# Kernel tuning notes

Measured on AMD Instinct MI355X. Metric: run time of the kernel, lower is better.

## Reference

```python
import jax, jax.numpy as jnp
import numpy as np

HEADS, DH, DIM = 16, 64, 1024
GAMMA, LAMBDA_REG = 0.01, 0.001


def _ln(x, g, b, eps=1e-5):
    mu = x.mean(-1, keepdims=True)
    var = x.var(-1, keepdims=True)  # biased var, matches torch LayerNorm
    return (x - mu) / jnp.sqrt(var + eps) * g + b


def setup_inputs() -> dict:
    key = jax.random.key(0)
    ks = jax.random.split(key, 8)
    B, NQ, NK = 8, 512, 512
    inner = HEADS * DH
    rn = lambda i, shp, sc: jax.random.normal(ks[i], shp, jnp.float32) * sc
    return {
        "q": rn(0, (B, NQ, DIM), 1.0),
        "k": rn(1, (B, NK, DIM), 1.0),
        "v": rn(2, (B, NK, DIM), 1.0),
        "ln_g": jnp.ones((DIM,), jnp.float32),
        "ln_b": jnp.zeros((DIM,), jnp.float32),
        "w_in": rn(3, (DIM, inner), 0.02),
        "wp_w1": rn(4, (2 * DH, DH), 0.05),
        "wp_b1": jnp.zeros((DH,), jnp.float32),
        "wp_lng": jnp.ones((DH,), jnp.float32),
        "wp_lnb": jnp.zeros((DH,), jnp.float32),
        "wp_w2": rn(5, (DH, DH // 2), 0.05),
        "wp_b2": jnp.zeros((DH // 2,), jnp.float32),
        "wp_w3": rn(6, (DH // 2, 3), 0.05),
        "wp_b3": jnp.zeros((3,), jnp.float32),
        "w_temp": jnp.ones((1,), jnp.float32) * 0.8,
        "w_out": rn(7, (inner, DIM), 0.02),
        "b_out": jnp.zeros((DIM,), jnp.float32),
    }


def reference(q, k, v, ln_g, ln_b, w_in, wp_w1, wp_b1, wp_lng, wp_lnb,
              wp_w2, wp_b2, wp_w3, wp_b3, w_temp, w_out, b_out):
    sg = jax.lax.stop_gradient

    def proj(x):  # input_linear (dropout=identity in eval) + head split
        y = _ln(x, ln_g, ln_b) @ w_in                      # [B,N,inner]
        B, N, _ = y.shape
        return y.reshape(B, N, HEADS, DH).transpose(2, 0, 1, 3)  # [h,B,N,d]

    f_q, f_k, f_v = proj(q), proj(k), proj(v)
    m = f_k.shape[2]
    eps = 1e-8

    # --- cosine component (clamp applied twice, as in source) ---
    dots = jnp.einsum('hbnd,hbmd->hbnm', f_q, f_k)
    n1 = jnp.linalg.norm(f_q, axis=-1, keepdims=True) + eps   # [h,B,Nq,1]
    n2 = jnp.linalg.norm(f_k, axis=-1, keepdims=True) + eps   # [h,B,Nk,1]
    cosine_sim = jnp.clip(dots / (n1 * jnp.swapaxes(n2, -1, -2)), -0.98, 0.98)

    # --- regularized covariance component ---
    f_kc = f_k - f_k.mean(axis=2, keepdims=True)
    f_qc = f_q - f_q.mean(axis=-1, keepdims=True)
    cov = jnp.einsum('hbnd,hbmd->hbnm', f_qc, f_kc) / (DH ** 0.5 + 1e-6)
    health = jnp.std(cov, ddof=1)
    base = LAMBDA_REG / max(m, 1)
    reg = jnp.where(health < 1e-5, base * 5.0,
                    jnp.where(health < 1e-3, base * 2.0, base))
    cov = jnp.clip(reg * cov, -25.0, 25.0)

    # --- margin-based variance component (eval: adaptive_gamma = gamma) ---
    fqn = f_q / jnp.maximum(jnp.linalg.norm(f_q, axis=-1, keepdims=True), 1e-6)
    fkn = f_k / jnp.maximum(jnp.linalg.norm(f_k, axis=-1, keepdims=True), 1e-6)
    cs = jnp.clip(jnp.einsum('hbnd,hbmd->hbnm', fqn, fkn), -0.98, 0.98)
    margin = jnp.clip(GAMMA - cs, 0.0, 5.0)
    var_c = jnp.broadcast_to(margin.mean(-1, keepdims=True), cs.shape)

    # --- dynamic per-head weight predictor MLP ---
    qk = jnp.concatenate([f_q.mean(axis=(1, 2)), f_k.mean(axis=(1, 2))], -1)  # [h,2d]
    h1 = jax.nn.relu(_ln(qk @ wp_w1 + wp_b1, wp_lng, wp_lnb))
    h2 = jax.nn.relu(h1 @ wp_w2 + wp_b2)
    logits = jax.nn.softmax(h2 @ wp_w3 + wp_b3, -1)  # MLP ends in Softmax
    temp = jnp.clip(w_temp, 0.1, 5.0)
    w = jax.nn.softmax(logits / temp, -1)            # second softmax with temp
    w = jnp.clip(w, 0.08, 0.75)
    w = w / w.sum(-1, keepdims=True)
    cw = w[:, 0].reshape(HEADS, 1, 1, 1)
    covw = w[:, 1].reshape(HEADS, 1, 1, 1)
    varw = w[:, 2].reshape(HEADS, 1, 1, 1)

    # --- health-based normalization (stds detached, as in source) ---
    cn = sg(jnp.std(cosine_sim, ddof=1)) + 1e-6
    covn = sg(jnp.std(cov, ddof=1)) + 1e-6
    varn = sg(jnp.std(var_c, ddof=1)) + 1e-6
    ch = jnp.minimum(cn, 1.0)
    covh = jnp.minimum(covn * 10.0, 1.0)
    varh = jnp.minimum(varn * 10.0, 1.0)
    dots_f = (cw * (cosine_sim / cn * ch)
              + covw * (cov / covn * 0.4 * covh)
              + varw * (var_c / varn * 0.4 * varh))

    # --- diversity-adaptive softmax temperature ---
    div = jnp.std(dots_f, ddof=1)
    atemp = jnp.where(div < 1e-5, 0.05, jnp.where(div < 1e-3, 0.2, 0.5 + div))
    atemp = jnp.clip(atemp, 0.05, 2.0)
    attn = jax.nn.softmax(dots_f / atemp, axis=-1)

    out = jnp.einsum('hbnm,hbmd->hbnd', attn, f_v)
    out = out.transpose(1, 2, 0, 3).reshape(q.shape[0], q.shape[1], HEADS * DH)
    return out @ w_out + b_out  # output_linear (dropout=identity)
```

## Files before the change

### kernel.cpp

```cpp
#include <hip/hip_runtime.h>
#include <math.h>

#define NHEADS 16
#define DHEAD  64
#define NDIM   1024
#define NB     8
#define NSEQ   512
#define NROWS  4096
#define NHB    128
#define NTOTD  33554432.0

typedef __bf16 bf16x8 __attribute__((ext_vector_type(8)));
typedef __bf16 bf16x4 __attribute__((ext_vector_type(4)));
typedef float  f32x4  __attribute__((ext_vector_type(4)));

#define MFMA(a,b,c) __builtin_amdgcn_mfma_f32_16x16x32_bf16(a,b,c,0,0,0)

static __device__ __forceinline__ size_t qk_off(int hbq, int n, int d){
  return ((size_t)hbq*32 + (n>>4))*1024 + (size_t)(d>>3)*128 + (size_t)(n&15)*8 + (d&7);
}

#define O_DSUMH  0
#define O_DSUME  1024
#define O_SCAL   2048
#define O_COEF   3072
#define O_W      4096
#define O_RQ1    131072
#define O_RQ2    393216
#define O_MQ     655360
#define O_QDMK   917504
#define O_RK1    1179648
#define O_RK2    1441792
#define O_KS2    1703936
#define O_MARG   1966080
#define O_RCS    2228224
#define O_RCOV   2490368
#define O_MK     2752512
#define O_QCOL   2785280
#define O_QHI    4194304
#define O_QLO    12582912
#define O_KHI    20971520
#define O_KLO    29360128
#define O_VTH    37748736
#define O_VTL    46137344
#define O_LNST   54525952
#define O_WTH    71303168
#define O_WTL    73400320
#define O_OUTH   75497472
#define O_OUTL   83886080
#define O_WOTH   92274688
#define O_WOTL   94371840

static __device__ __forceinline__ float clamp98(float x){ return fminf(fmaxf(x,-0.98f),0.98f); }

__global__ __launch_bounds__(256) void ln_stats_kernel(const float* __restrict__ q,
    const float* __restrict__ k, const float* __restrict__ v, float* __restrict__ st){
  int row = blockIdx.x, t = threadIdx.x;
  const float* x = (blockIdx.y==0) ? q : (blockIdx.y==1 ? k : v);
  float4 vv = *(const float4*)(x + (size_t)row*1024 + t*4);
  float s  = vv.x+vv.y+vv.z+vv.w;
  float ss = vv.x*vv.x+vv.y*vv.y+vv.z*vv.z+vv.w*vv.w;
  for (int off=32; off; off>>=1){ s += __shfl_down(s,off); ss += __shfl_down(ss,off); }
  __shared__ float sh[8];
  if ((t&63)==0){ sh[t>>6]=s; sh[4+(t>>6)]=ss; }
  __syncthreads();
  if (t==0){
    float S=sh[0]+sh[1]+sh[2]+sh[3], SS=sh[4]+sh[5]+sh[6]+sh[7];
    float mu = S*(1.0f/1024.0f);
    st[blockIdx.y*8192 + row*2]   = mu;
    st[blockIdx.y*8192 + row*2+1] = 1.0f/sqrtf(SS*(1.0f/1024.0f) - mu*mu + 1e-5f);
  }
}

__global__ __launch_bounds__(256) void transpose_split_kernel(const float* __restrict__ wsrc,
    __bf16* __restrict__ th, __bf16* __restrict__ tl){
  __shared__ float tile[64][65];
  int k0 = blockIdx.x*64, n0 = blockIdx.y*64;
  int t = threadIdx.x;
  int c = t&63, r4 = t>>6;
  #pragma unroll
  for (int i=0;i<16;i++){
    int kr = r4 + i*4;
    tile[kr][c] = wsrc[(size_t)(k0+kr)*1024 + n0 + c];
  }
  __syncthreads();
  #pragma unroll
  for (int i=0;i<16;i++){
    int nr = r4 + i*4;
    float v = tile[c][nr];
    __bf16 hv = (__bf16)v;
    size_t o = (size_t)(n0+nr)*1024 + k0 + c;
    th[o] = hv; tl[o] = (__bf16)(v - (float)hv);
  }
}

__global__ __launch_bounds__(256) void proj_gemm_kernel(
  const float* __restrict__ q, const float* __restrict__ k, const float* __restrict__ v,
  const float* __restrict__ lnst0,
  const float* __restrict__ gv, const float* __restrict__ bv,
  const __bf16* __restrict__ Bth, const __bf16* __restrict__ Btl,
  __bf16* __restrict__ qhi, __bf16* __restrict__ qlo,
  __bf16* __restrict__ khi, __bf16* __restrict__ klo,
  __bf16* __restrict__ vth, __bf16* __restrict__ vtl)
{
  __shared__ __bf16 Ash[128][68];
  __shared__ __bf16 Asl[128][68];
  __shared__ __bf16 Bsh[64][68];
  __shared__ __bf16 Bsl[64][68];
  int z = blockIdx.z;
  const float* X = (z==0)? q : (z==1? k : v);
  const float* lnst = lnst0 + z*8192;
  __bf16* oh = (z==0)? qhi : (z==1? khi : vth);
  __bf16* ol = (z==0)? qlo : (z==1? klo : vtl);
  int t = threadIdx.x, w = t>>6, lane = t&63, lr = lane&15, lq = lane>>4;
  int vid = blockIdx.y*16 + blockIdx.x;
  int cX = vid&7, r2 = vid>>3;
  int ytile = cX*4 + (r2>>4);
  int xtile = r2&15;
  int rbase = ytile*128;
  int cbase = xtile*64;
  int wr = w>>1, wc = w&1;
  int srow = t>>3;
  int scol = (t&7)*8;
  f32x4 acc[4][2] = {};
  for (int kt=0; kt<16; kt++){
    int k0 = kt*64;
    bf16x8 va[4], vA[4], vb[2], vB[2];
    float4 g0 = *(const float4*)(gv + k0 + scol);
    float4 g1 = *(const float4*)(gv + k0 + scol + 4);
    float4 b0 = *(const float4*)(bv + k0 + scol);
    float4 b1 = *(const float4*)(bv + k0 + scol + 4);
    #pragma unroll
    for (int r=0;r<4;r++){
      int row = rbase + r*32 + srow;
      size_t gi = (size_t)row*1024 + k0 + scol;
      float4 x0 = *(const float4*)(X + gi);
      float4 x1 = *(const float4*)(X + gi + 4);
      float mu = lnst[row*2], rs = lnst[row*2+1];
      float o[8];
      o[0]=(x0.x-mu)*rs*g0.x+b0.x; o[1]=(x0.y-mu)*rs*g0.y+b0.y;
      o[2]=(x0.z-mu)*rs*g0.z+b0.z; o[3]=(x0.w-mu)*rs*g0.w+b0.w;
      o[4]=(x1.x-mu)*rs*g1.x+b1.x; o[5]=(x1.y-mu)*rs*g1.y+b1.y;
      o[6]=(x1.z-mu)*rs*g1.z+b1.z; o[7]=(x1.w-mu)*rs*g1.w+b1.w;
      bf16x8 hv, lv;
      #pragma unroll
      for (int e=0;e<8;e++){
        __bf16 hb_ = (__bf16)o[e];
        hv[e] = hb_; lv[e] = (__bf16)(o[e]-(float)hb_);
      }
      va[r]=hv; vA[r]=lv;
    }
    #pragma unroll
    for (int r=0;r<2;r++){
      size_t gi = (size_t)(cbase + r*32 + srow)*1024 + k0 + scol;
      vb[r] = *(const bf16x8*)(Bth + gi);
      vB[r] = *(const bf16x8*)(Btl + gi);
    }
    #pragma unroll
    for (int r=0;r<4;r++){
      *(bf16x8*)&Ash[r*32+srow][scol] = va[r];
      *(bf16x8*)&Asl[r*32+srow][scol] = vA[r];
    }
    #pragma unroll
    for (int r=0;r<2;r++){
      *(bf16x8*)&Bsh[r*32+srow][scol] = vb[r];
      *(bf16x8*)&Bsl[r*32+srow][scol] = vB[r];
    }
    __syncthreads();
    #pragma unroll
    for (int kc=0; kc<2; kc++){
      int ko = kc*32 + lq*8;
      bf16x8 ah[4], al[4], bh[2], bl[2];
      #pragma unroll
      for (int i=0;i<4;i++){
        ah[i] = *(const bf16x8*)&Ash[wr*64 + i*16 + lr][ko];
        al[i] = *(const bf16x8*)&Asl[wr*64 + i*16 + lr][ko];
      }
      #pragma unroll
      for (int j=0;j<2;j++){
        bh[j] = *(const bf16x8*)&Bsh[wc*32 + j*16 + lr][ko];
        bl[j] = *(const bf16x8*)&Bsl[wc*32 + j*16 + lr][ko];
      }
      #pragma unroll
      for (int i=0;i<4;i++)
        #pragma unroll
        for (int j=0;j<2;j++){
          acc[i][j] = MFMA(al[i], bh[j], acc[i][j]);
          acc[i][j] = MFMA(ah[i], bl[j], acc[i][j]);
          acc[i][j] = MFMA(ah[i], bh[j], acc[i][j]);
        }
    }
    __syncthreads();
  }
  #pragma unroll
  for (int i=0;i<4;i++)
    #pragma unroll
    for (int j=0;j<2;j++)
      #pragma unroll
      for (int r=0;r<4;r++){
        int row = rbase + wr*64 + i*16 + lq*4 + r;
        int col = cbase + wc*32 + j*16 + lr;
        float val = acc[i][j][r];
        __bf16 hv = (__bf16)val;
        __bf16 lv = (__bf16)(val - (float)hv);
        int n = row & 511, b2 = row >> 9;
        int hh = col >> 6, d = col & 63;
        int hbq = hh*8 + b2;
        size_t o;
        if (z<2){
          o = qk_off(hbq, n, d);
        } else {
          o = (((size_t)hbq*4 + (d>>4))*16 + (n>>5))*512
            + (size_t)((((n>>3)&3)*16) + (d&15))*8 + (n&7);
        }
        oh[o] = hv; ol[o] = lv;
      }
}

__global__ __launch_bounds__(256) void final_gemm_kernel(
  const __bf16* __restrict__ Ah, const __bf16* __restrict__ Al,
  const __bf16* __restrict__ Bth, const __bf16* __restrict__ Btl,
  const float* __restrict__ bias, float* __restrict__ of)
{
  __shared__ __bf16 Ash[128][68];
  __shared__ __bf16 Asl[128][68];
  __shared__ __bf16 Bsh[64][68];
  __shared__ __bf16 Bsl[64][68];
  int t = threadIdx.x, w = t>>6, lane = t&63, lr = lane&15, lq = lane>>4;
  int vid = blockIdx.y*16 + blockIdx.x;
  int cX = vid&7, r2 = vid>>3;
  int ytile = cX*4 + (r2>>4);
  int xtile = r2&15;
  int rbase = ytile*128;
  int cbase = xtile*64;
  int wr = w>>1, wc = w&1;
  int srow = t>>3;
  int scol = (t&7)*8;
  f32x4 acc[4][2] = {};
  for (int kt=0; kt<16; kt++){
    int k0 = kt*64;
    bf16x8 va[4], vA[4], vb[2], vB[2];
    #pragma unroll
    for (int r=0;r<4;r++){
      size_t gi = (size_t)(rbase + r*32 + srow)*1024 + k0 + scol;
      va[r] = *(const bf16x8*)(Ah + gi);
      vA[r] = *(const bf16x8*)(Al + gi);
    }
    #pragma unroll
    for (int r=0;r<2;r++){
      size_t gi = (size_t)(cbase + r*32 + srow)*1024 + k0 + scol;
      vb[r] = *(const bf16x8*)(Bth + gi);
      vB[r] = *(const bf16x8*)(Btl + gi);
    }
    #pragma unroll
    for (int r=0;r<4;r++){
      *(bf16x8*)&Ash[r*32+srow][scol] = va[r];
      *(bf16x8*)&Asl[r*32+srow][scol] = vA[r];
    }
    #pragma unroll
    for (int r=0;r<2;r++){
      *(bf16x8*)&Bsh[r*32+srow][scol] = vb[r];
      *(bf16x8*)&Bsl[r*32+srow][scol] = vB[r];
    }
    __syncthreads();
    #pragma unroll
    for (int kc=0; kc<2; kc++){
      int ko = kc*32 + lq*8;
      bf16x8 ah[4], al[4], bh[2], bl[2];
      #pragma unroll
      for (int i=0;i<4;i++){
        ah[i] = *(const bf16x8*)&Ash[wr*64 + i*16 + lr][ko];
        al[i] = *(const bf16x8*)&Asl[wr*64 + i*16 + lr][ko];
      }
      #pragma unroll
      for (int j=0;j<2;j++){
        bh[j] = *(const bf16x8*)&Bsh[wc*32 + j*16 + lr][ko];
        bl[j] = *(const bf16x8*)&Bsl[wc*32 + j*16 + lr][ko];
      }
      #pragma unroll
      for (int i=0;i<4;i++)
        #pragma unroll
        for (int j=0;j<2;j++){
          acc[i][j] = MFMA(al[i], bh[j], acc[i][j]);
          acc[i][j] = MFMA(ah[i], bl[j], acc[i][j]);
          acc[i][j] = MFMA(ah[i], bh[j], acc[i][j]);
        }
    }
    __syncthreads();
  }
  #pragma unroll
  for (int i=0;i<4;i++)
    #pragma unroll
    for (int j=0;j<2;j++)
      #pragma unroll
      for (int r=0;r<4;r++){
        int row = rbase + wr*64 + i*16 + lq*4 + r;
        int col = cbase + wc*32 + j*16 + lr;
        of[(size_t)row*1024 + col] = acc[i][j][r] + bias[col];
      }
}

__global__ void kstats_kernel(const __bf16* __restrict__ kh, const __bf16* __restrict__ kl,
    float* __restrict__ mk, float* __restrict__ rk1, float* __restrict__ rk2, float* __restrict__ ks2){
  int hb = blockIdx.x;
  size_t base = (size_t)hb*32768;
  int t = threadIdx.x;
  __shared__ float csA[32][64];
  __shared__ float mks_lds[64];
  __shared__ float mksum_sh;
  int c2 = t&7, mg = t>>3;
  float fs[8] = {};
  for (int m=mg; m<512; m+=32){
    size_t off = base + (size_t)(m>>4)*1024 + c2*128 + (size_t)(m&15)*8;
    bf16x8 h = *(const bf16x8*)(kh+off);
    bf16x8 l = *(const bf16x8*)(kl+off);
    #pragma unroll
    for (int e=0;e<8;e++) fs[e] += (float)h[e]+(float)l[e];
  }
  #pragma unroll
  for (int e=0;e<8;e++) csA[mg][c2*8+e] = fs[e];
  __syncthreads();
  if (t<64){
    float s=0;
    #pragma unroll
    for (int g=0;g<32;g++) s += csA[g][t];
    float vv = s*(1.0f/512.0f);
    mk[hb*64+t] = vv;
    mks_lds[t] = vv;
  }
  __syncthreads();
  if (t==0){
    float s=0;
    for (int i=0;i<64;i++) s += mks_lds[i];
    mksum_sh = s;
  }
  __syncthreads();
  float mks = mksum_sh;
  int l8 = t&7, rg = t>>3;
  for (int m=rg; m<512; m+=32){
    size_t off = base + (size_t)(m>>4)*1024 + l8*128 + (size_t)(m&15)*8;
    bf16x8 h = *(const bf16x8*)(kh+off);
    bf16x8 l = *(const bf16x8*)(kl+off);
    float s=0, ss=0;
    #pragma unroll
    for (int e=0;e<8;e++){ float vv=(float)h[e]+(float)l[e]; s+=vv; ss+=vv*vv; }
    for (int o2=4;o2;o2>>=1){ s+=__shfl_xor(s,o2); ss+=__shfl_xor(ss,o2); }
    if (l8==0){
      float nk = sqrtf(ss);
      rk1[hb*512+m] = 1.0f/(nk+1e-8f);
      rk2[hb*512+m] = 1.0f/fmaxf(nk,1e-6f);
      ks2[hb*512+m] = s - mks;
    }
  }
}

__global__ void qstats_kernel(const __bf16* __restrict__ qh, const __bf16* __restrict__ ql,
    const float* __restrict__ mk, float* __restrict__ rq1, float* __restrict__ rq2,
    float* __restrict__ mq, float* __restrict__ qdotmk, float* __restrict__ qcol){
  int hb = blockIdx.x;
  size_t base = (size_t)hb*32768;
  int t = threadIdx.x;
  __shared__ float csA[32][64];
  __shared__ float mks_lds[64];
  int c2 = t&7, mg = t>>3;
  if (t<64) mks_lds[t] = mk[hb*64+t];
  float fs[8] = {};
  for (int m=mg; m<512; m+=32){
    size_t off = base + (size_t)(m>>4)*1024 + c2*128 + (size_t)(m&15)*8;
    bf16x8 h = *(const bf16x8*)(qh+off);
    bf16x8 l = *(const bf16x8*)(ql+off);
    #pragma unroll
    for (int e=0;e<8;e++) fs[e] += (float)h[e]+(float)l[e];
  }
  #pragma unroll
  for (int e=0;e<8;e++) csA[mg][c2*8+e] = fs[e];
  __syncthreads();
  if (t<64){
    float s=0;
    #pragma unroll
    for (int g=0;g<32;g++) s += csA[g][t];
    qcol[hb*64+t] = s;
  }
  int l8 = t&7, rg = t>>3;
  float mkv[8];
  #pragma unroll
  for (int e=0;e<8;e++) mkv[e] = mks_lds[l8*8+e];
  for (int n=rg; n<512; n+=32){
    size_t off = base + (size_t)(n>>4)*1024 + l8*128 + (size_t)(n&15)*8;
    bf16x8 h = *(const bf16x8*)(qh+off);
    bf16x8 l = *(const bf16x8*)(ql+off);
    float s=0, ss=0, qd=0;
    #pragma unroll
    for (int e=0;e<8;e++){
      float vv=(float)h[e]+(float)l[e];
      s+=vv; ss+=vv*vv; qd+=vv*mkv[e];
    }
    for (int o2=4;o2;o2>>=1){ s+=__shfl_xor(s,o2); ss+=__shfl_xor(ss,o2); qd+=__shfl_xor(qd,o2); }
    if (l8==0){
      float nq = sqrtf(ss);
      rq1[hb*512+n] = 1.0f/(nq+1e-8f);
      rq2[hb*512+n] = 1.0f/fmaxf(nq,1e-6f);
      mq[hb*512+n]  = s*(1.0f/64.0f);
      qdotmk[hb*512+n] = qd;
    }
  }
}

__global__ void mlp_kernel(const float* __restrict__ qcol, const float* __restrict__ mk,
   const float* __restrict__ w1, const float* __restrict__ b1, const float* __restrict__ lng,
   const float* __restrict__ lnb, const float* __restrict__ w2, const float* __restrict__ b2,
   const float* __restrict__ w3, const float* __restrict__ b3, const float* __restrict__ wtemp,
   float* __restrict__ W){
  int h = blockIdx.x;
  int j = threadIdx.x;
  __shared__ float qk[128], h1[64], h2[32];
  float sq=0, sk=0;
  #pragma unroll
  for (int b=0;b<8;b++){
    sq += qcol[(h*8+b)*64 + j];
    sk += mk[(h*8+b)*64 + j];
  }
  qk[j]    = sq*(1.0f/4096.0f);
  qk[64+j] = sk*(1.0f/8.0f);
  __syncthreads();
  float a = b1[j];
  for (int i=0;i<128;i++) a += qk[i]*w1[i*64+j];
  float s=a, ss=a*a;
  for (int off=32; off; off>>=1){ s += __shfl_xor(s,off); ss += __shfl_xor(ss,off); }
  float mu = s*(1.0f/64.0f), var = ss*(1.0f/64.0f)-mu*mu;
  float v = (a-mu)/sqrtf(var+1e-5f)*lng[j] + lnb[j];
  h1[j] = fmaxf(v, 0.0f);
  __syncthreads();
  if (j<32){
    float a2 = b2[j];
    for (int i=0;i<64;i++) a2 += h1[i]*w2[i*32+j];
    h2[j] = fmaxf(a2,0.0f);
  }
  __syncthreads();
  if (j==0){
    float l[3];
    for (int kq=0;kq<3;kq++){ float a3=b3[kq]; for(int i=0;i<32;i++) a3 += h2[i]*w3[i*3+kq]; l[kq]=a3; }
    float m = fmaxf(l[0],fmaxf(l[1],l[2]));
    float e0=expf(l[0]-m), e1=expf(l[1]-m), e2=expf(l[2]-m);
    float si = 1.0f/(e0+e1+e2);
    float temp = fminf(fmaxf(wtemp[0], 0.1f), 5.0f);
    float t0=e0*si/temp, t1=e1*si/temp, t2=e2*si/temp;
    float m2 = fmaxf(t0,fmaxf(t1,t2));
    float f0=expf(t0-m2), f1=expf(t1-m2), f2=expf(t2-m2);
    float s2i = 1.0f/(f0+f1+f2);
    float wv[3] = {f0*s2i, f1*s2i, f2*s2i};
    float wsum=0.0f;
    for (int kq=0;kq<3;kq++){ wv[kq]=fminf(fmaxf(wv[kq],0.08f),0.75f); wsum+=wv[kq]; }
    for (int kq=0;kq<3;kq++) W[h*3+kq] = wv[kq]/wsum;
  }
}

__global__ __launch_bounds__(256) void s1_mfma_kernel(
  const __bf16* __restrict__ qhp, const __bf16* __restrict__ qlp,
  const __bf16* __restrict__ khp, const __bf16* __restrict__ klp,
  const float* __restrict__ rq1, const float* __restrict__ rq2,
  const float* __restrict__ mq, const float* __restrict__ qdmk,
  const float* __restrict__ rk1, const float* __restrict__ rk2,
  const float* __restrict__ ks2,
  double* __restrict__ dsumH, float* __restrict__ margin,
  float* __restrict__ rcs, float* __restrict__ rcov)
{
  int vid = blockIdx.y*8 + blockIdx.x;
  int cX = vid&7, r2 = vid>>3;
  int hb = cX*16 + (r2>>3);
  int n0 = (r2&7)*64;
  size_t qb = (size_t)hb*32768;
  __shared__ float sm[512][3];
  __shared__ float sn[64][4];
  int t = threadIdx.x;
  for (int mm=t; mm<512; mm+=256){
    int m = hb*512 + mm;
    sm[mm][0]=rk1[m]; sm[mm][1]=rk2[m]; sm[mm][2]=ks2[m];
  }
  if (t<64){
    int n = hb*512 + n0 + t;
    sn[t][0]=rq1[n]; sn[t][1]=rq2[n]; sn[t][2]=mq[n]; sn[t][3]=qdmk[n];
  }
  __syncthreads();
  int w = t>>6, lane = t&63, lr = lane&15, lq = lane>>4;
  int nw = w*16;
  float lcs=0,lcs2=0,lcov=0,lcov2=0,lcscov=0;
  float mrow[4]={}, csr[4]={}, cvr[4]={};
  float nr1[4],nr2[4],nmq[4],nqd[4];
  #pragma unroll
  for (int r=0;r<4;r++){
    int nl = nw + lq*4 + r;
    nr1[r]=sn[nl][0]; nr2[r]=sn[nl][1]; nmq[r]=sn[nl][2]; nqd[r]=sn[nl][3];
  }
  for (int mc=0; mc<4; mc++){
    int m0 = mc*128;
    f32x4 acc[8] = {};
    #pragma unroll
    for (int kc=0; kc<2; kc++){
      size_t qoff = qb + (size_t)((n0+nw)>>4)*1024 + kc*512 + (size_t)lane*8;
      bf16x8 ah = *(const bf16x8*)(qhp + qoff);
      bf16x8 al = *(const bf16x8*)(qlp + qoff);
      #pragma unroll
      for (int j=0;j<8;j++){
        size_t off = qb + (size_t)((m0>>4)+j)*1024 + kc*512 + (size_t)lane*8;
        bf16x8 bh = *(const bf16x8*)(khp + off);
        bf16x8 bl = *(const bf16x8*)(klp + off);
        acc[j] = MFMA(ah, bh, acc[j]);
        acc[j] = MFMA(ah, bl, acc[j]);
        acc[j] = MFMA(al, bh, acc[j]);
      }
    }
    #pragma unroll
    for (int j=0;j<8;j++){
      int ml = m0 + j*16 + lr;
      float k1=sm[ml][0], k2=sm[ml][1], ksv=sm[ml][2];
      #pragma unroll
      for (int r=0;r<4;r++){
        float dv = acc[j][r];
        float cs = clamp98(dv*nr1[r]*k1);
        float c2 = clamp98(dv*nr2[r]*k2);
        float mg = fminf(fmaxf(0.01f-c2,0.0f),5.0f);
        float cv = dv - nqd[r] - nmq[r]*ksv;
        lcs+=cs; lcs2+=cs*cs; lcov+=cv; lcov2+=cv*cv; lcscov+=cs*cv;
        mrow[r]+=mg; csr[r]+=cs; cvr[r]+=cv;
      }
    }
  }
  for (int off=1; off<16; off<<=1)
    #pragma unroll
    for (int r=0;r<4;r++){
      mrow[r]+=__shfl_xor(mrow[r],off);
      csr[r] +=__shfl_xor(csr[r],off);
      cvr[r]+=__shfl_xor(cvr[r],off);
    }
  if (lr==0){
    #pragma unroll
    for (int r=0;r<4;r++){
      int n = hb*512 + n0 + nw + lq*4 + r;
      margin[n] = mrow[r]*(1.0f/512.0f);
      rcs[n]    = csr[r];
      rcov[n]   = cvr[r];
    }
  }
  for (int off=32; off; off>>=1){
    lcs+=__shfl_xor(lcs,off); lcs2+=__shfl_xor(lcs2,off);
    lcov+=__shfl_xor(lcov,off); lcov2+=__shfl_xor(lcov2,off);
    lcscov+=__shfl_xor(lcscov,off);
  }
  __shared__ double red[4][5];
  if (lane==0){ red[w][0]=lcs; red[w][1]=lcs2; red[w][2]=lcov; red[w][3]=lcov2; red[w][4]=lcscov; }
  __syncthreads();
  if (t==0){
    int h = hb>>3;
    for (int c=0;c<5;c++)
      atomicAdd(&dsumH[h*5+c], red[0][c]+red[1][c]+red[2][c]+red[3][c]);
  }
}

__global__ void margfin_kernel(const float* __restrict__ margin, double* __restrict__ dsumE){
  double s=0, ss=0;
  for (int k2=0;k2<4;k2++){
    int idx = blockIdx.x*1024 + k2*256 + threadIdx.x;
    float v = margin[idx];
    s += v; ss += (double)v*v;
  }
  for (int off=32; off; off>>=1){ s+=__shfl_down(s,off); ss+=__shfl_down(ss,off); }
  __shared__ double sh[8];
  int t = threadIdx.x;
  if ((t&63)==0){ sh[t>>6]=s; sh[4+(t>>6)]=ss; }
  __syncthreads();
  if (t==0){
    atomicAdd(dsumE+0, sh[0]+sh[1]+sh[2]+sh[3]);
    atomicAdd(dsumE+1, sh[4]+sh[5]+sh[6]+sh[7]);
  }
}

__global__ void scalars1_kernel(const double* __restrict__ dsumH, double* __restrict__ dsumE,
                                const float* __restrict__ W, float* __restrict__ coef){
  double Scs=0,Scs2=0,Scov=0,Scov2=0;
  for (int h=0;h<16;h++){
    Scs += dsumH[h*5+0]; Scs2 += dsumH[h*5+1];
    Scov += dsumH[h*5+2]; Scov2 += dsumH[h*5+3];
  }
  double N = NTOTD;
  double cn = sqrt(fmax((Scs2-Scs*Scs/N)/(N-1.0),0.0)) + 1e-6;
  double ch = fmin(cn, 1.0);
  const double covscale = 1.0/8.000001;
  double sc_ = Scov*covscale, sc2_ = Scov2*covscale*covscale;
  double health = sqrt(fmax((sc2_-sc_*sc_/N)/(N-1.0),0.0));
  double base = 0.001/512.0;
  double reg = health<1e-5 ? base*5.0 : (health<1e-3 ? base*2.0 : base);
  double covn = reg*health + 1e-6;
  double covh = fmin(covn*10.0, 1.0);
  double vs = dsumE[0]*512.0, vs2 = dsumE[1]*512.0;
  double varn = sqrt(fmax((vs2 - vs*vs/N)/(N-1.0),0.0)) + 1e-6;
  double varh = fmin(varn*10.0, 1.0);
  double sdf=0, sdf2=0;
  for (int h=0;h<16;h++){
    double cC  = (double)W[h*3+0]*ch/cn;
    double cCv = (double)W[h*3+1]*reg*covscale*0.4*covh/covn;
    double cVr = (double)W[h*3+2]*0.4*varh/varn;
    coef[h*3+0] = (float)cC;
    coef[h*3+1] = (float)cCv;
    coef[h*3+2] = (float)cVr;
    sdf  += cC*dsumH[h*5+0] + cCv*dsumH[h*5+2];
    sdf2 += cC*cC*dsumH[h*5+1] + cCv*cCv*dsumH[h*5+3] + 2.0*cC*cCv*dsumH[h*5+4];
  }
  dsumE[2] = sdf;
  dsumE[3] = sdf2;
}

__global__ void rowfold_kernel(const float* __restrict__ margin, const float* __restrict__ rcs,
                               const float* __restrict__ rcov, const float* __restrict__ coef,
                               double* __restrict__ dsumE){
  int idx = blockIdx.x*256 + threadIdx.x;
  int h = idx >> 12;
  float cC = coef[h*3+0], cCv = coef[h*3+1], cVr = coef[h*3+2];
  float vc = cVr * margin[idx];
  double s0 = 512.0*(double)vc;
  double s1 = 2.0*(double)vc*((double)cC*(double)rcs[idx] + (double)cCv*(double)rcov[idx])
            + 512.0*(double)vc*(double)vc;
  for (int off=32; off; off>>=1){ s0+=__shfl_down(s0,off); s1+=__shfl_down(s1,off); }
  __shared__ double sh[8];
  int t = threadIdx.x;
  if ((t&63)==0){ sh[t>>6]=s0; sh[4+(t>>6)]=s1; }
  __syncthreads();
  if (t==0){
    atomicAdd(dsumE+2, sh[0]+sh[1]+sh[2]+sh[3]);
    atomicAdd(dsumE+3, sh[4]+sh[5]+sh[6]+sh[7]);
  }
}

__global__ void scalars2_kernel(const double* __restrict__ dsumE, float* __restrict__ scal){
  double N = NTOTD;
  double div = sqrt(fmax((dsumE[3]-dsumE[2]*dsumE[2]/N)/(N-1.0),0.0));
  double at = div<1e-5 ? 0.05 : (div<1e-3 ? 0.2 : 0.5+div);
  at = fmin(fmax(at,0.05),2.0);
  scal[0] = (float)(1.0/at);
}

#define PSTRIDE 536
__global__ __launch_bounds__(512) void s3_mfma_kernel(
  const __bf16* __restrict__ qhp, const __bf16* __restrict__ qlp,
  const __bf16* __restrict__ khp, const __bf16* __restrict__ klp,
  const __bf16* __restrict__ vth, const __bf16* __restrict__ vtl,
  const float* __restrict__ rq1, const float* __restrict__ mq,
  const float* __restrict__ qdmk, const float* __restrict__ rk1,
  const float* __restrict__ ks2, const float* __restrict__ margin,
  const float* __restrict__ coef, const float* __restrict__ scal,
  __bf16* __restrict__ outh, __bf16* __restrict__ outl)
{
  int vid = blockIdx.y*16 + blockIdx.x;
  int cX = vid&7, r2 = vid>>3;
  int hb = cX*16 + (r2>>4);
  int n0 = (r2&15)*32;
  int h = hb>>3, b = hb&7;
  size_t qb = (size_t)hb*32768;

  __shared__ unsigned short Plds[32][PSTRIDE];
  __shared__ float nst[32][4];
  __shared__ float mst[512][2];
  __shared__ float pmax[32][8];
  __shared__ float psum[32][8];

  int t = threadIdx.x, w = t>>6, lane = t&63, lr = lane&15, lq = lane>>4;
  if (t<32){
    int n = hb*512 + n0 + t;
    nst[t][0] = rq1[n]; nst[t][1] = mq[n]; nst[t][2] = qdmk[n];
    nst[t][3] = coef[h*3+2]*margin[n];
  }
  {
    int m = hb*512 + t;
    mst[t][0] = rk1[m]; mst[t][1] = ks2[m];
  }
  float cC = coef[h*3+0], cCv = coef[h*3+1];
  float invat = scal[0];
  __syncthreads();

  int ms0 = w*64;
  f32x4 acc[2][4] = {};
  #pragma unroll
  for (int kc=0; kc<2; kc++){
    bf16x8 qhf[2], qlf[2];
    #pragma unroll
    for (int i=0;i<2;i++){
      size_t off = qb + (size_t)((n0>>4)+i)*1024 + kc*512 + (size_t)lane*8;
      qhf[i] = *(const bf16x8*)(qhp + off);
      qlf[i] = *(const bf16x8*)(qlp + off);
    }
    #pragma unroll
    for (int j=0;j<4;j++){
      size_t off = qb + (size_t)((ms0>>4)+j)*1024 + kc*512 + (size_t)lane*8;
      bf16x8 khf = *(const bf16x8*)(khp + off);
      bf16x8 klf = *(const bf16x8*)(klp + off);
      #pragma unroll
      for (int i=0;i<2;i++){
        acc[i][j] = MFMA(qlf[i], khf, acc[i][j]);
        acc[i][j] = MFMA(qhf[i], klf, acc[i][j]);
        acc[i][j] = MFMA(qhf[i], khf, acc[i][j]);
      }
    }
  }
  float rmax[2][4];
  #pragma unroll
  for (int i=0;i<2;i++){
    float a0[4],a1[4],a2[4],a3[4];
    #pragma unroll
    for (int r=0;r<4;r++){
      int nl = i*16 + lq*4 + r;
      a0[r]=nst[nl][0]; a1[r]=nst[nl][1]; a2[r]=nst[nl][2]; a3[r]=nst[nl][3];
      rmax[i][r] = -1e30f;
    }
    #pragma unroll
    for (int j=0;j<4;j++){
      int m = ms0 + j*16 + lr;
      float k1 = mst[m][0], ksv = mst[m][1];
      #pragma unroll
      for (int r=0;r<4;r++){
        float dv = acc[i][j][r];
        float cs = clamp98(dv*a0[r]*k1);
        float covr = dv - a2[r] - a1[r]*ksv;
        float df = cC*cs + cCv*covr + a3[r];
        acc[i][j][r] = df;
        rmax[i][r] = fmaxf(rmax[i][r], df);
      }
    }
  }
  #pragma unroll
  for (int i=0;i<2;i++)
    #pragma unroll
    for (int r=0;r<4;r++)
      for (int off=1; off<16; off<<=1)
        rmax[i][r] = fmaxf(rmax[i][r], __shfl_xor(rmax[i][r], off));
  if (lr==0){
    #pragma unroll
    for (int i=0;i<2;i++)
      #pragma unroll
      for (int r=0;r<4;r++)
        pmax[i*16+lq*4+r][w] = rmax[i][r];
  }
  __syncthreads();
  float rsum[2][4] = {};
  #pragma unroll
  for (int i=0;i<2;i++){
    float Mf[4];
    #pragma unroll
    for (int r=0;r<4;r++){
      int nl = i*16+lq*4+r;
      float m0_ = fmaxf(fmaxf(pmax[nl][0],pmax[nl][1]),fmaxf(pmax[nl][2],pmax[nl][3]));
      float m1_ = fmaxf(fmaxf(pmax[nl][4],pmax[nl][5]),fmaxf(pmax[nl][6],pmax[nl][7]));
      Mf[r] = fmaxf(m0_,m1_);
    }
    #pragma unroll
    for (int j=0;j<4;j++){
      int m = ms0 + j*16 + lr;
      #pragma unroll
      for (int r=0;r<4;r++){
        float p = __expf((acc[i][j][r]-Mf[r])*invat);
        rsum[i][r] += p;
        *(__bf16*)&Plds[i*16+lq*4+r][m] = (__bf16)p;
      }
    }
  }
  #pragma unroll
  for (int i=0;i<2;i++)
    #pragma unroll
    for (int r=0;r<4;r++)
      for (int off=1; off<16; off<<=1)
        rsum[i][r] += __shfl_xor(rsum[i][r], off);
  if (lr==0){
    #pragma unroll
    for (int i=0;i<2;i++)
      #pragma unroll
      for (int r=0;r<4;r++)
        psum[i*16+lq*4+r][w] = rsum[i][r];
  }
  __syncthreads();

  int rt = (w&1)*16;
  int dtg = w>>1;
  f32x4 acc2 = {};
  for (int kc=0; kc<16; kc++){
    bf16x8 pa = *(const bf16x8*)&Plds[rt+lr][kc*32 + lq*8];
    size_t vi = (((size_t)hb*4 + dtg)*16 + kc)*512 + (size_t)lane*8;
    bf16x8 vh = *(const bf16x8*)(vth + vi);
    bf16x8 vl = *(const bf16x8*)(vtl + vi);
    acc2 = MFMA(pa, vl, acc2);
    acc2 = MFMA(pa, vh, acc2);
  }
  float rsinv[4];
  #pragma unroll
  for (int r=0;r<4;r++){
    int nl = rt + lq*4 + r;
    float s0_ = psum[nl][0]+psum[nl][1]+psum[nl][2]+psum[nl][3];
    float s1_ = psum[nl][4]+psum[nl][5]+psum[nl][6]+psum[nl][7];
    rsinv[r] = 1.0f/(s0_+s1_);
  }
  #pragma unroll
  for (int r=0;r<4;r++){
    float o = acc2[r]*rsinv[r];
    int rowg = b*512 + n0 + rt + lq*4 + r;
    int colg = h*64 + dtg*16 + lr;
    size_t oi = (size_t)rowg*1024 + colg;
    __bf16 hv = (__bf16)o;
    outh[oi] = hv;
    outl[oi] = (__bf16)(o - (float)hv);
  }
}

extern "C" void kernel_launch(void* const* d_in, const int* in_sizes, int n_in,
                              void* d_out, int out_size, void* d_ws, size_t ws_size,
                              hipStream_t stream) {
  (void)in_sizes; (void)n_in; (void)out_size; (void)ws_size;
  const float* q     = (const float*)d_in[0];
  const float* k     = (const float*)d_in[1];
  const float* v     = (const float*)d_in[2];
  const float* ln_g  = (const float*)d_in[3];
  const float* ln_b  = (const float*)d_in[4];
  const float* w_in  = (const float*)d_in[5];
  const float* wp_w1 = (const float*)d_in[6];
  const float* wp_b1 = (const float*)d_in[7];
  const float* wp_lng= (const float*)d_in[8];
  const float* wp_lnb= (const float*)d_in[9];
  const float* wp_w2 = (const float*)d_in[10];
  const float* wp_b2 = (const float*)d_in[11];
  const float* wp_w3 = (const float*)d_in[12];
  const float* wp_b3 = (const float*)d_in[13];
  const float* w_temp= (const float*)d_in[14];
  const float* w_out = (const float*)d_in[15];
  const float* b_out = (const float*)d_in[16];

  char* ws = (char*)d_ws;
  double* dsumH = (double*)(ws + O_DSUMH);
  double* dsumE = (double*)(ws + O_DSUME);
  float* scal  = (float*)(ws + O_SCAL);
  float* coef  = (float*)(ws + O_COEF);
  float* W     = (float*)(ws + O_W);
  float* rq1   = (float*)(ws + O_RQ1);
  float* rq2   = (float*)(ws + O_RQ2);
  float* mqp   = (float*)(ws + O_MQ);
  float* qdmk  = (float*)(ws + O_QDMK);
  float* rk1   = (float*)(ws + O_RK1);
  float* rk2   = (float*)(ws + O_RK2);
  float* ks2   = (float*)(ws + O_KS2);
  float* marg  = (float*)(ws + O_MARG);
  float* rcs   = (float*)(ws + O_RCS);
  float* rcov  = (float*)(ws + O_RCOV);
  float* mk    = (float*)(ws + O_MK);
  float* qcol  = (float*)(ws + O_QCOL);
  float* lnst  = (float*)(ws + O_LNST);
  __bf16* qhi  = (__bf16*)(ws + O_QHI);
  __bf16* qlo  = (__bf16*)(ws + O_QLO);
  __bf16* khi  = (__bf16*)(ws + O_KHI);
  __bf16* klo  = (__bf16*)(ws + O_KLO);
  __bf16* vth  = (__bf16*)(ws + O_VTH);
  __bf16* vtl  = (__bf16*)(ws + O_VTL);
  __bf16* wth  = (__bf16*)(ws + O_WTH);
  __bf16* wtl  = (__bf16*)(ws + O_WTL);
  __bf16* outh = (__bf16*)(ws + O_OUTH);
  __bf16* outl = (__bf16*)(ws + O_OUTL);
  __bf16* woth = (__bf16*)(ws + O_WOTH);
  __bf16* wotl = (__bf16*)(ws + O_WOTL);
  float* outf  = (float*)d_out;

  hipMemsetAsync(ws + O_DSUMH, 0, 2048, stream);

  transpose_split_kernel<<<dim3(16,16),256,0,stream>>>(w_in,  wth, wtl);
  transpose_split_kernel<<<dim3(16,16),256,0,stream>>>(w_out, woth, wotl);
  ln_stats_kernel<<<dim3(4096,3),256,0,stream>>>(q, k, v, lnst);

  proj_gemm_kernel<<<dim3(16,32,3),256,0,stream>>>(q, k, v, lnst, ln_g, ln_b, wth, wtl,
                                                   qhi, qlo, khi, klo, vth, vtl);

  kstats_kernel<<<128,256,0,stream>>>(khi, klo, mk, rk1, rk2, ks2);
  qstats_kernel<<<128,256,0,stream>>>(qhi, qlo, mk, rq1, rq2, mqp, qdmk, qcol);
  mlp_kernel<<<16,64,0,stream>>>(qcol,mk,wp_w1,wp_b1,wp_lng,wp_lnb,wp_w2,wp_b2,wp_w3,wp_b3,w_temp,W);

  s1_mfma_kernel<<<dim3(8,128),256,0,stream>>>(qhi,qlo,khi,klo,rq1,rq2,mqp,qdmk,rk1,rk2,ks2,
                                               dsumH,marg,rcs,rcov);
  margfin_kernel<<<64,256,0,stream>>>(marg, dsumE);
  scalars1_kernel<<<1,1,0,stream>>>(dsumH, dsumE, W, coef);
  rowfold_kernel<<<256,256,0,stream>>>(marg, rcs, rcov, coef, dsumE);
  scalars2_kernel<<<1,1,0,stream>>>(dsumE, scal);

  s3_mfma_kernel<<<dim3(16,128),512,0,stream>>>(qhi,qlo,khi,klo,vth,vtl,
                                                rq1,mqp,qdmk,rk1,ks2,marg,coef,scal,outh,outl);
  final_gemm_kernel<<<dim3(16,32),256,0,stream>>>(outh, outl, woth, wotl, b_out, outf);
}
```

Baseline: 335.3 us.

## Register-prefetch next K tile in projection and output GEMMs; merge weight transposes

Both the projection GEMM and the output GEMM now load the next K-tile of A and B from global memory into registers right after the barrier, so those loads overlap the MFMA work on the current shared-memory tile. The projection GEMM also hoists the per-row LayerNorm mean and inverse std out of the K loop. The two weight transpose/split launches are merged into one launch using blockIdx.z. This raises register pressure, which could lower occupancy.

```diff
diff --git a/kernel.cpp b/kernel.cpp
--- a/kernel.cpp
+++ b/kernel.cpp
@@ -72,8 +72,13 @@
   }
 }
 
-__global__ __launch_bounds__(256) void transpose_split_kernel(const float* __restrict__ wsrc,
-    __bf16* __restrict__ th, __bf16* __restrict__ tl){
+__global__ __launch_bounds__(256) void transpose_split_kernel(
+    const float* __restrict__ w0, const float* __restrict__ w1,
+    __bf16* __restrict__ th0, __bf16* __restrict__ tl0,
+    __bf16* __restrict__ th1, __bf16* __restrict__ tl1){
+  const float* wsrc = blockIdx.z ? w1 : w0;
+  __bf16* th = blockIdx.z ? th1 : th0;
+  __bf16* tl = blockIdx.z ? tl1 : tl0;
   __shared__ float tile[64][65];
   int k0 = blockIdx.x*64, n0 = blockIdx.y*64;
   int t = threadIdx.x;
@@ -122,51 +127,71 @@
   int wr = w>>1, wc = w&1;
   int srow = t>>3;
   int scol = (t&7)*8;
+  float muv[4], rsv[4];
+  #pragma unroll
+  for (int r=0;r<4;r++){
+    int row = rbase + r*32 + srow;
+    muv[r] = lnst[row*2]; rsv[r] = lnst[row*2+1];
+  }
   f32x4 acc[4][2] = {};
+  float4 xlo[4], xhi[4];
+  bf16x8 pb[2], pB[2];
+  #pragma unroll
+  for (int r=0;r<4;r++){
+    size_t gi = (size_t)(rbase + r*32 + srow)*1024 + scol;
+    xlo[r] = *(const float4*)(X + gi);
+    xhi[r] = *(const float4*)(X + gi + 4);
+  }
+  #pragma unroll
+  for (int r=0;r<2;r++){
+    size_t gi = (size_t)(cbase + r*32 + srow)*1024 + scol;
+    pb[r] = *(const bf16x8*)(Bth + gi);
+    pB[r] = *(const bf16x8*)(Btl + gi);
+  }
   for (int kt=0; kt<16; kt++){
     int k0 = kt*64;
-    bf16x8 va[4], vA[4], vb[2], vB[2];
     float4 g0 = *(const float4*)(gv + k0 + scol);
     float4 g1 = *(const float4*)(gv + k0 + scol + 4);
     float4 b0 = *(const float4*)(bv + k0 + scol);
     float4 b1 = *(const float4*)(bv + k0 + scol + 4);
     #pragma unroll
     for (int r=0;r<4;r++){
-      int row = rbase + r*32 + srow;
-      size_t gi = (size_t)row*1024 + k0 + scol;
-      float4 x0 = *(const float4*)(X + gi);
-      float4 x1 = *(const float4*)(X + gi + 4);
-      float mu = lnst[row*2], rs = lnst[row*2+1];
+      float mu = muv[r], rs = rsv[r];
       float o[8];
-      o[0]=(x0.x-mu)*rs*g0.x+b0.x; o[1]=(x0.y-mu)*rs*g0.y+b0.y;
-      o[2]=(x0.z-mu)*rs*g0.z+b0.z; o[3]=(x0.w-mu)*rs*g0.w+b0.w;
-      o[4]=(x1.x-mu)*rs*g1.x+b1.x; o[5]=(x1.y-mu)*rs*g1.y+b1.y;
-      o[6]=(x1.z-mu)*rs*g1.z+b1.z; o[7]=(x1.w-mu)*rs*g1.w+b1.w;
+      o[0]=(xlo[r].x-mu)*rs*g0.x+b0.x; o[1]=(xlo[r].y-mu)*rs*g0.y+b0.y;
+      o[2]=(xlo[r].z-mu)*rs*g0.z+b0.z; o[3]=(xlo[r].w-mu)*rs*g0.w+b0.w;
+      o[4]=(xhi[r].x-mu)*rs*g1.x+b1.x; o[5]=(xhi[r].y-mu)*rs*g1.y+b1.y;
+      o[6]=(xhi[r].z-mu)*rs*g1.z+b1.z; o[7]=(xhi[r].w-mu)*rs*g1.w+b1.w;
       bf16x8 hv, lv;
       #pragma unroll
       for (int e=0;e<8;e++){
         __bf16 hb_ = (__bf16)o[e];
         hv[e] = hb_; lv[e] = (__bf16)(o[e]-(float)hb_);
       }
-      va[r]=hv; vA[r]=lv;
+      *(bf16x8*)&Ash[r*32+srow][scol] = hv;
+      *(bf16x8*)&Asl[r*32+srow][scol] = lv;
     }
     #pragma unroll
     for (int r=0;r<2;r++){
-      size_t gi = (size_t)(cbase + r*32 + srow)*1024 + k0 + scol;
-      vb[r] = *(const bf16x8*)(Bth + gi);
-      vB[r] = *(const bf16x8*)(Btl + gi);
-    }
-    #pragma unroll
-    for (int r=0;r<4;r++){
-      *(bf16x8*)&Ash[r*32+srow][scol] = va[r];
-      *(bf16x8*)&Asl[r*32+srow][scol] = vA[r];
-    }
-    #pragma unroll
-    for (int r=0;r<2;r++){
-      *(bf16x8*)&Bsh[r*32+srow][scol] = vb[r];
-      *(bf16x8*)&Bsl[r*32+srow][scol] = vB[r];
+      *(bf16x8*)&Bsh[r*32+srow][scol] = pb[r];
+      *(bf16x8*)&Bsl[r*32+srow][scol] = pB[r];
     }
     __syncthreads();
+    if (kt<15){
+      int k1 = k0 + 64;
+      #pragma unroll
+      for (int r=0;r<4;r++){
+        size_t gi = (size_t)(rbase + r*32 + srow)*1024 + k1 + scol;
+        xlo[r] = *(const float4*)(X + gi);
+        xhi[r] = *(const float4*)(X + gi + 4);
+      }
+      #pragma unroll
+      for (int r=0;r<2;r++){
+        size_t gi = (size_t)(cbase + r*32 + srow)*1024 + k1 + scol;
+        pb[r] = *(const bf16x8*)(Bth + gi);
+        pB[r] = *(const bf16x8*)(Btl + gi);
+      }
+    }
     #pragma unroll
     for (int kc=0; kc<2; kc++){
       int ko = kc*32 + lq*8;
@@ -237,32 +262,47 @@
   int srow = t>>3;
   int scol = (t&7)*8;
   f32x4 acc[4][2] = {};
+  bf16x8 pa[4], pA[4], pb[2], pB[2];
+  #pragma unroll
+  for (int r=0;r<4;r++){
+    size_t gi = (size_t)(rbase + r*32 + srow)*1024 + scol;
+    pa[r] = *(const bf16x8*)(Ah + gi);
+    pA[r] = *(const bf16x8*)(Al + gi);
+  }
+  #pragma unroll
+  for (int r=0;r<2;r++){
+    size_t gi = (size_t)(cbase + r*32 + srow)*1024 + scol;
+    pb[r] = *(const bf16x8*)(Bth + gi);
+    pB[r] = *(const bf16x8*)(Btl + gi);
+  }
   for (int kt=0; kt<16; kt++){
     int k0 = kt*64;
-    bf16x8 va[4], vA[4], vb[2], vB[2];
     #pragma unroll
     for (int r=0;r<4;r++){
-      size_t gi = (size_t)(rbase + r*32 + srow)*1024 + k0 + scol;
-      va[r] = *(const bf16x8*)(Ah + gi);
-      vA[r] = *(const bf16x8*)(Al + gi);
+      *(bf16x8*)&Ash[r*32+srow][scol] = pa[r];
+      *(bf16x8*)&Asl[r*32+srow][scol] = pA[r];
     }
     #pragma unroll
     for (int r=0;r<2;r++){
-      size_t gi = (size_t)(cbase + r*32 + srow)*1024 + k0 + scol;
-      vb[r] = *(const bf16x8*)(Bth + gi);
-      vB[r] = *(const bf16x8*)(Btl + gi);
-    }
-    #pragma unroll
-    for (int r=0;r<4;r++){
-      *(bf16x8*)&Ash[r*32+srow][scol] = va[r];
-      *(bf16x8*)&Asl[r*32+srow][scol] = vA[r];
-    }
-    #pragma unroll
-    for (int r=0;r<2;r++){
-      *(bf16x8*)&Bsh[r*32+srow][scol] = vb[r];
-      *(bf16x8*)&Bsl[r*32+srow][scol] = vB[r];
+      *(bf16x8*)&Bsh[r*32+srow][scol] = pb[r];
+      *(bf16x8*)&Bsl[r*32+srow][scol] = pB[r];
     }
     __syncthreads();
+    if (kt<15){
+      int k1 = k0 + 64;
+      #pragma unroll
+      for (int r=0;r<4;r++){
+        size_t gi = (size_t)(rbase + r*32 + srow)*1024 + k1 + scol;
+        pa[r] = *(const bf16x8*)(Ah + gi);
+        pA[r] = *(const bf16x8*)(Al + gi);
+      }
+      #pragma unroll
+      for (int r=0;r<2;r++){
+        size_t gi = (size_t)(cbase + r*32 + srow)*1024 + k1 + scol;
+        pb[r] = *(const bf16x8*)(Bth + gi);
+        pB[r] = *(const bf16x8*)(Btl + gi);
+      }
+    }
     #pragma unroll
     for (int kc=0; kc<2; kc++){
       int ko = kc*32 + lq*8;
@@ -865,8 +905,7 @@
 
   hipMemsetAsync(ws + O_DSUMH, 0, 2048, stream);
 
-  transpose_split_kernel<<<dim3(16,16),256,0,stream>>>(w_in,  wth, wtl);
-  transpose_split_kernel<<<dim3(16,16),256,0,stream>>>(w_out, woth, wotl);
+  transpose_split_kernel<<<dim3(16,16,2),256,0,stream>>>(w_in, w_out, wth, wtl, woth, wotl);
   ln_stats_kernel<<<dim3(4096,3),256,0,stream>>>(q, k, v, lnst);
 
   proj_gemm_kernel<<<dim3(16,32,3),256,0,stream>>>(q, k, v, lnst, ln_g, ln_b, wth, wtl,
```

After: 323.7 us (median of 2 runs). -3.5%, faster.
